# Performance work log

Measured on AMD Instinct MI355X. Metric: run time of the kernel, lower is better.

Reference implementation:

```python
import jax, jax.numpy as jnp
import numpy as np

TEMPERATURE = 0.1
TOPK = 64


def setup_inputs() -> dict:
    key = jax.random.key(0)
    heatmap = jax.random.normal(key, (2, 16, 96, 128, 128), dtype=jnp.float32)
    return {"heatmap": heatmap}


def reference(heatmap) -> jnp.ndarray:
    B, C, D, H, W = heatmap.shape
    heat_flat = heatmap.reshape(B, C, D * H * W)
    k = min(TOPK, D * H * W)

    # top-k over flattened volume per (batch, channel)
    values, indices = jax.lax.top_k(heat_flat, k)  # [B, C, k]

    # temperature softmax over the k selected values (matches torch: exp-sum + 1e-20 eps)
    w = values / TEMPERATURE
    w = w - jnp.max(w, axis=-1, keepdims=True)
    ew = jnp.exp(w)
    probs = ew / (jnp.sum(ew, axis=-1, keepdims=True) + 1e-20)  # [B, C, k]

    # Decode voxel coordinates from flat indices (equivalent to gathering from the
    # meshgrid coords_flat table): coord order is (d, h, w) == (x, y, z) in the original.
    d = (indices // (H * W)).astype(jnp.float32)
    h = ((indices % (H * W)) // W).astype(jnp.float32)
    wv = (indices % W).astype(jnp.float32)
    selected_coords = jnp.stack([d, h, wv], axis=-1)  # [B, C, k, 3]

    # soft-argmax: probability-weighted coordinate sum
    weighted_coords = jnp.sum(probs[..., None] * selected_coords, axis=2)  # [B, C, 3]
    return weighted_coords
```

## Files before the change

### kernel.cpp

```cpp
#include <hip/hip_runtime.h>
#include <stdint.h>

#define ROWS 32
#define ROWLEN (96*128*128)
#define SEG 1024
#define SEGS_PER_ROW (ROWLEN / SEG)
#define NSEG_TOTAL (ROWS * SEGS_PER_ROW)
#define SEGS_PER_WAVE 6
#define NWAVES (NSEG_TOTAL / SEGS_PER_WAVE)
#define NBLOCKS_SCAN (NWAVES / 4)
#define NGROUPS 64
#define GRPSZ (SEGS_PER_ROW / NGROUPS)
#define CAP 8192
#define HW_ (128*128)
#define W_ 128

__global__ __launch_bounds__(256) void scan_kernel(const float4* __restrict__ in,
                                                   float* __restrict__ segMax) {
    const int wid  = (blockIdx.x * 256 + threadIdx.x) >> 6;
    const int lane = threadIdx.x & 63;
    const int s0 = wid * SEGS_PER_WAVE;

    #pragma unroll
    for (int t = 0; t < SEGS_PER_WAVE; ++t) {
        const float4* p = in + (size_t)(s0 + t) * (SEG/4) + lane;
        float4 a = p[0], b = p[64], c = p[128], d = p[192];
        float m = fmaxf(fmaxf(fmaxf(a.x, a.y), fmaxf(a.z, a.w)),
                        fmaxf(fmaxf(b.x, b.y), fmaxf(b.z, b.w)));
        m = fmaxf(m, fmaxf(fmaxf(c.x, c.y), fmaxf(c.z, c.w)));
        m = fmaxf(m, fmaxf(fmaxf(d.x, d.y), fmaxf(d.z, d.w)));
        #pragma unroll
        for (int off = 32; off; off >>= 1) m = fmaxf(m, __shfl_xor(m, off));
        if (lane == 0) segMax[s0 + t] = m;
    }
}

__global__ __launch_bounds__(1024) void select_kernel(const float4* __restrict__ in,
                                                      const float* __restrict__ segMax,
                                                      float* __restrict__ out) {
    const int row = blockIdx.x;
    const int tid = threadIdx.x;
    const int wav = tid >> 6, lane = tid & 63;

    __shared__ float sm[SEGS_PER_ROW];
    __shared__ int   surv[SEGS_PER_ROW];
    __shared__ int   nSurv, nCand;
    __shared__ float Tsh;
    __shared__ float candV[CAP];
    __shared__ int   candI[CAP];
    __shared__ float topV[64];
    __shared__ int   topI[64];

    for (int i = tid; i < SEGS_PER_ROW; i += 1024)
        sm[i] = segMax[(size_t)row * SEGS_PER_ROW + i];
    if (tid == 0) { nSurv = 0; nCand = 0; }
    __syncthreads();

    if (tid < NGROUPS) {
        float m = -INFINITY;
        #pragma unroll
        for (int j = 0; j < GRPSZ; ++j) m = fmaxf(m, sm[tid * GRPSZ + j]);
        #pragma unroll
        for (int off = 32; off; off >>= 1) m = fminf(m, __shfl_xor(m, off));
        if (tid == 0) Tsh = m;
    }
    __syncthreads();
    const float T = Tsh;

    for (int i = tid; i < SEGS_PER_ROW; i += 1024)
        if (sm[i] >= T) { int p = atomicAdd(&nSurv, 1); surv[p] = i; }
    __syncthreads();

    const int ns = nSurv;
    for (int si = wav; si < ns; si += 16) {
        const int s = surv[si];
        const float4* p = in + ((size_t)row * SEGS_PER_ROW + s) * (SEG/4) + lane;
        #pragma unroll
        for (int j = 0; j < 4; ++j) {
            float4 q = p[j * 64];
            float a[4] = {q.x, q.y, q.z, q.w};
            #pragma unroll
            for (int c = 0; c < 4; ++c) {
                if (a[c] >= T) {
                    int pos = atomicAdd(&nCand, 1);
                    if (pos < CAP) {
                        candV[pos] = a[c];
                        candI[pos] = s * SEG + (j * 64 + lane) * 4 + c;
                    }
                }
            }
        }
    }
    __syncthreads();
    int n = nCand; if (n > CAP) n = CAP;

    for (int i = tid; i < n; i += 1024) {
        const float vi = candV[i];
        const int   ii = candI[i];
        int rank = 0;
        for (int j = 0; j < n; ++j) {
            const float vj = candV[j];
            rank += (vj > vi) || (vj == vi && candI[j] < ii);
        }
        if (rank < 64) { topV[rank] = vi; topI[rank] = ii; }
    }
    __syncthreads();

    if (tid < 64) {
        const float v = topV[tid];
        const int idx = topI[tid];
        float m = v;
        #pragma unroll
        for (int off = 32; off; off >>= 1) m = fmaxf(m, __shfl_xor(m, off));
        const float e = expf((v - m) * 10.0f);
        const float fd = (float)(idx / HW_);
        const int rem = idx % HW_;
        const float fh = (float)(rem / W_);
        const float fw = (float)(rem % W_);
        float se = e, sd = e * fd, sh = e * fh, sw = e * fw;
        #pragma unroll
        for (int off = 32; off; off >>= 1) {
            se += __shfl_xor(se, off);
            sd += __shfl_xor(sd, off);
            sh += __shfl_xor(sh, off);
            sw += __shfl_xor(sw, off);
        }
        if (tid == 0) {
            const float inv = 1.0f / (se + 1e-20f);
            out[row * 3 + 0] = sd * inv;
            out[row * 3 + 1] = sh * inv;
            out[row * 3 + 2] = sw * inv;
        }
    }
}

extern "C" void kernel_launch(void* const* d_in, const int* in_sizes, int n_in,
                              void* d_out, int out_size, void* d_ws, size_t ws_size,
                              hipStream_t stream) {
    const float* heat = (const float*)d_in[0];
    float* out = (float*)d_out;
    float* segMax = (float*)d_ws;

    hipLaunchKernelGGL(scan_kernel, dim3(NBLOCKS_SCAN), dim3(256), 0, stream,
                       (const float4*)heat, segMax);
    hipLaunchKernelGGL(select_kernel, dim3(ROWS), dim3(1024), 0, stream,
                       (const float4*)heat, segMax, out);
}
```

Measured before the change: 344.9 us.

## Record per-segment top-2 and index to skip rescanning single-candidate segments

The scan kernel now tracks each segment's max, second max and argmax, and writes all three to workspace. The select kernel adds a segment directly as one candidate when only its max clears the threshold, and rereads only segments holding two or more candidates. This cuts the serial re-read of global memory done by only 32 blocks in the select phase. In exchange the scan does more per-element compare/branch work, its loop over segments is no longer unrolled, and it writes three arrays instead of one.

```diff
diff --git a/kernel.cpp b/kernel.cpp
--- a/kernel.cpp
+++ b/kernel.cpp
@@ -16,31 +16,53 @@
 #define W_ 128
 
 __global__ __launch_bounds__(256) void scan_kernel(const float4* __restrict__ in,
-                                                   float* __restrict__ segMax) {
+                                                   float* __restrict__ segMax,
+                                                   float* __restrict__ segMax2,
+                                                   int* __restrict__ segIdx) {
     const int wid  = (blockIdx.x * 256 + threadIdx.x) >> 6;
     const int lane = threadIdx.x & 63;
     const int s0 = wid * SEGS_PER_WAVE;
 
-    #pragma unroll
     for (int t = 0; t < SEGS_PER_WAVE; ++t) {
-        const float4* p = in + (size_t)(s0 + t) * (SEG/4) + lane;
-        float4 a = p[0], b = p[64], c = p[128], d = p[192];
-        float m = fmaxf(fmaxf(fmaxf(a.x, a.y), fmaxf(a.z, a.w)),
-                        fmaxf(fmaxf(b.x, b.y), fmaxf(b.z, b.w)));
-        m = fmaxf(m, fmaxf(fmaxf(c.x, c.y), fmaxf(c.z, c.w)));
-        m = fmaxf(m, fmaxf(fmaxf(d.x, d.y), fmaxf(d.z, d.w)));
+        const int s = s0 + t;
+        const float4* p = in + (size_t)s * (SEG/4) + lane;
+        float m1 = -INFINITY, m2 = -INFINITY;
+        int i1 = 0;
         #pragma unroll
-        for (int off = 32; off; off >>= 1) m = fmaxf(m, __shfl_xor(m, off));
-        if (lane == 0) segMax[s0 + t] = m;
+        for (int j = 0; j < 4; ++j) {
+            float4 q = p[j * 64];
+            float a[4] = {q.x, q.y, q.z, q.w};
+            #pragma unroll
+            for (int c = 0; c < 4; ++c) {
+                const float v = a[c];
+                const int idx = (j * 64 + lane) * 4 + c;
+                if (v > m1)      { m2 = m1; m1 = v; i1 = idx; }
+                else if (v > m2) { m2 = v; }
+            }
+        }
+        #pragma unroll
+        for (int off = 32; off; off >>= 1) {
+            const float o1 = __shfl_xor(m1, off);
+            const float o2 = __shfl_xor(m2, off);
+            const int   oi = __shfl_xor(i1, off);
+            const float n2 = fmaxf(fminf(m1, o1), fmaxf(m2, o2));
+            const bool  gt = (o1 > m1) || (o1 == m1 && oi < i1);
+            if (gt) { m1 = o1; i1 = oi; }
+            m2 = n2;
+        }
+        if (lane == 0) { segMax[s] = m1; segMax2[s] = m2; segIdx[s] = i1; }
     }
 }
 
 __global__ __launch_bounds__(1024) void select_kernel(const float4* __restrict__ in,
                                                       const float* __restrict__ segMax,
+                                                      const float* __restrict__ segMax2,
+                                                      const int* __restrict__ segIdx,
                                                       float* __restrict__ out) {
     const int row = blockIdx.x;
     const int tid = threadIdx.x;
     const int wav = tid >> 6, lane = tid & 63;
+    const int base = row * SEGS_PER_ROW;
 
     __shared__ float sm[SEGS_PER_ROW];
     __shared__ int   surv[SEGS_PER_ROW];
@@ -52,7 +74,7 @@
     __shared__ int   topI[64];
 
     for (int i = tid; i < SEGS_PER_ROW; i += 1024)
-        sm[i] = segMax[(size_t)row * SEGS_PER_ROW + i];
+        sm[i] = segMax[base + i];
     if (tid == 0) { nSurv = 0; nCand = 0; }
     __syncthreads();
 
@@ -67,14 +89,26 @@
     __syncthreads();
     const float T = Tsh;
 
-    for (int i = tid; i < SEGS_PER_ROW; i += 1024)
-        if (sm[i] >= T) { int p = atomicAdd(&nSurv, 1); surv[p] = i; }
+    for (int i = tid; i < SEGS_PER_ROW; i += 1024) {
+        if (sm[i] >= T) {
+            if (segMax2[base + i] < T) {
+                int p = atomicAdd(&nCand, 1);
+                if (p < CAP) {
+                    candV[p] = sm[i];
+                    candI[p] = i * SEG + segIdx[base + i];
+                }
+            } else {
+                int p = atomicAdd(&nSurv, 1);
+                surv[p] = i;
+            }
+        }
+    }
     __syncthreads();
 
     const int ns = nSurv;
     for (int si = wav; si < ns; si += 16) {
         const int s = surv[si];
-        const float4* p = in + ((size_t)row * SEGS_PER_ROW + s) * (SEG/4) + lane;
+        const float4* p = in + ((size_t)base + s) * (SEG/4) + lane;
         #pragma unroll
         for (int j = 0; j < 4; ++j) {
             float4 q = p[j * 64];
@@ -139,10 +173,14 @@
                               hipStream_t stream) {
     const float* heat = (const float*)d_in[0];
     float* out = (float*)d_out;
-    float* segMax = (float*)d_ws;
+
+    uint8_t* base = (uint8_t*)d_ws;
+    float* segMax  = (float*)(base);
+    float* segMax2 = (float*)(base + 196608);
+    int*   segIdx  = (int*)(base + 393216);
 
     hipLaunchKernelGGL(scan_kernel, dim3(NBLOCKS_SCAN), dim3(256), 0, stream,
-                       (const float4*)heat, segMax);
+                       (const float4*)heat, segMax, segMax2, segIdx);
     hipLaunchKernelGGL(select_kernel, dim3(ROWS), dim3(1024), 0, stream,
-                       (const float4*)heat, segMax, out);
+                       (const float4*)heat, segMax, segMax2, segIdx, out);
 }
```

New measurement: 309.0 us. 10.4% less time.
